# Kernel optimization log

Hardware: AMD Instinct MI355X
Metric: run time of the kernel (lower is better)

## Reference

```python
import jax, jax.numpy as jnp
import numpy as np

N = 4096
IN_C = 256
F = 256          # num_filter
C = 40           # label_dim
KP1 = 3          # K+1 Chebyshev orders (K=2 hardcoded in forward)
E = 131072
TWO_PI = 2.0 * np.pi


def build_Lc(edges, q, edge_weight, n):
    """Conjugate of the normalized magnetic Laplacian (max_eigen=2 => L = -A_n * exp(i*Theta)).
    We return conj(L) because the original code swaps L.real/L.imag when feeding `process`,
    which is algebraically O_i = i * conj(T_i(L))."""
    row, col = edges[0], edges[1]
    A = jnp.zeros((n, n), jnp.float32).at[row, col].add(edge_weight)  # duplicates sum, as in coo_matrix
    A_sym = 0.5 * (A + A.T)
    d = A_sym.sum(axis=0)
    d = jnp.where(d == 0, 1.0, d)
    dinv = d ** -0.5
    A_n = dinv[:, None] * A_sym * dinv[None, :]
    Theta = TWO_PI * q * (A - A.T)
    # conj(L) = -A_n * exp(-i*Theta)
    return (-A_n).astype(jnp.complex64) * jnp.exp(-1j * Theta.astype(jnp.complex64))


def cheb_layer(Lc, Xr, Xi, W, b):
    """One ChebConv_Qin_Direct layer. Output = sum_i (i * T_i(conj(L)) @ Xc) @ W_i + bias,
    which reproduces the real/imag-swapped `process` of the original module."""
    Xc = (Xr + 1j * Xi).astype(jnp.complex64)      # [N, d]
    Z0 = Xc
    Z1 = Lc @ Xc                                   # sparse-equivalent spmm, dense here
    Z2 = 2.0 * (Lc @ Z1) - Z0                      # Chebyshev recursion T2 = 2 L T1 - T0
    Yc = 1j * (Z0 @ W[0].astype(jnp.complex64)
               + Z1 @ W[1].astype(jnp.complex64)
               + Z2 @ W[2].astype(jnp.complex64))  # [N, out]
    return Yc.real + b, Yc.imag + b


def setup_inputs() -> dict:
    key = jax.random.key(0)
    k = jax.random.split(key, 8)
    stdv1 = 1.0 / np.sqrt(F)
    return {
        "real": jax.random.normal(k[0], (N, IN_C), jnp.float32),
        "imag": jax.random.normal(k[1], (N, IN_C), jnp.float32),
        "edges": jax.random.randint(k[2], (2, E), 0, N),
        "q": jnp.float32(0.25),
        "edge_weight": jax.random.uniform(k[3], (E,), jnp.float32),
        "W1": jax.random.uniform(k[4], (KP1, IN_C, F), jnp.float32, -stdv1, stdv1),
        "b1": jnp.zeros((1, F), jnp.float32),
        "W2": jax.random.uniform(k[5], (KP1, F, F), jnp.float32, -stdv1, stdv1),
        "b2": jnp.zeros((1, F), jnp.float32),
        "Wc": jax.random.normal(k[6], (C, 2 * F), jnp.float32) * (1.0 / np.sqrt(2 * F)),
        "bc": jnp.zeros((C,), jnp.float32),
    }


def reference(real, imag, edges, q, edge_weight, W1, b1, W2, b2, Wc, bc):
    n = real.shape[0]
    Lc = build_Lc(edges, q, edge_weight, n)        # same L is rebuilt each layer in the original
    r, i = cheb_layer(Lc, real, imag, W1, b1)
    r, i = cheb_layer(Lc, r, i, W2, b2)            # activation=False, dropout=False
    x = jnp.concatenate([r, i], axis=-1)           # [N, 2F]
    logits = x @ Wc.T + bc                         # Conv1d(kernel_size=1) == linear
    return jax.nn.log_softmax(logits, axis=-1)     # [N, C]
```

## Files before the change

### kernel.cpp

```cpp
#include <hip/hip_runtime.h>
#include <cmath>

#define N_NODES 4096
#define FDIM    256
#define CDIM    40
#define NEDGE   131072
#define CAP     256
#define HBITS   20
#define HSIZE   (1 << HBITS)
#define TWO_PI_F 6.28318530717958647692f

typedef __bf16 bf16;
typedef __bf16 bf16x2 __attribute__((ext_vector_type(2)));
typedef __bf16 bf16x4 __attribute__((ext_vector_type(4)));
typedef __bf16 bf16x8 __attribute__((ext_vector_type(8)));
typedef float  f32x4  __attribute__((ext_vector_type(4)));

static constexpr size_t NF = (size_t)N_NODES * FDIM;

struct __align__(16) Entry { float lr, li; int col, pad; };

__device__ __forceinline__ void gld_lds16(const bf16* g, bf16* s) {
    __builtin_amdgcn_global_load_lds(
        (const __attribute__((address_space(1))) void*)g,
        (__attribute__((address_space(3))) void*)s,
        16, 0, 0);
}

__device__ __forceinline__ unsigned cell_hash(unsigned cell) {
    return (cell * 2654435761u) >> (32 - HBITS);
}

__global__ void hash_insert(const int* __restrict__ edges,
                            const float* __restrict__ ew,
                            int* __restrict__ hkey, float* __restrict__ hval,
                            float* __restrict__ rowsum, float* __restrict__ colsum) {
    int e = blockIdx.x * blockDim.x + threadIdx.x;
    if (e >= NEDGE) return;
    int r = edges[e], c = edges[NEDGE + e];
    float wv = ew[e];
    atomicAdd(rowsum + r, wv);
    atomicAdd(colsum + c, wv);
    unsigned cell = (unsigned)r * N_NODES + c;
    unsigned h = cell_hash(cell);
    for (;;) {
        int old = atomicCAS(hkey + h, 0, (int)(cell + 1));
        if (old == 0 || old == (int)(cell + 1)) { atomicAdd(hval + h, wv); break; }
        h = (h + 1) & (HSIZE - 1);
    }
}

__global__ void dinv_k(const float* __restrict__ rowsum,
                       const float* __restrict__ colsum,
                       float* __restrict__ dinv) {
    int j = blockIdx.x * blockDim.x + threadIdx.x;
    if (j < N_NODES) {
        float d = 0.5f * (rowsum[j] + colsum[j]);
        if (d == 0.f) d = 1.f;
        dinv[j] = 1.0f / sqrtf(d);
    }
}

__global__ __launch_bounds__(256) void hash_to_ell(
    const int* __restrict__ hkey, const float* __restrict__ hval,
    const float* __restrict__ dinv, const float* __restrict__ qptr,
    int* __restrict__ cnt, Entry* __restrict__ ent) {
    int h = blockIdx.x * 256 + threadIdx.x;
    int k = hkey[h];
    if (k == 0) return;
    unsigned cell = (unsigned)(k - 1);
    int i = cell >> 12, j = cell & 4095;
    float a = hval[h];
    float b = 0.f;
    bool mirror = false;
    if (i == j) { b = a; mirror = true; }
    else {
        unsigned mcell = (unsigned)j * N_NODES + i;
        unsigned hh = cell_hash(mcell);
        for (;;) {
            int kk = hkey[hh];
            if (kk == (int)(mcell + 1)) { b = hval[hh]; mirror = true; break; }
            if (kk == 0) break;
            hh = (hh + 1) & (HSIZE - 1);
        }
    }
    float an = 0.5f * (a + b) * dinv[i] * dinv[j];
    float s, c;
    sincosf(TWO_PI_F * qptr[0] * (a - b), &s, &c);
    int pos = atomicAdd(cnt + i, 1);
    if (pos < CAP) {
        Entry en; en.lr = -an * c; en.li = an * s; en.col = j; en.pad = 0;
        ent[(size_t)i * CAP + pos] = en;
    }
    if (!mirror) {
        int pos2 = atomicAdd(cnt + j, 1);
        if (pos2 < CAP) {
            Entry en; en.lr = -an * c; en.li = -an * s; en.col = i; en.pad = 0;
            ent[(size_t)j * CAP + pos2] = en;
        }
    }
}

__global__ __launch_bounds__(256) void cast_in2(const float* __restrict__ Xr,
                                                const float* __restrict__ Xi,
                                                bf16* __restrict__ Xr16,
                                                bf16* __restrict__ Xi16,
                                                bf16* __restrict__ XC) {
    int idx = blockIdx.x * 256 + threadIdx.x;
    float vr = Xr[idx], vi = Xi[idx];
    Xr16[idx] = (bf16)vr; Xi16[idx] = (bf16)vi;
    bf16x2 p; p[0] = (bf16)vr; p[1] = (bf16)vi;
    ((bf16x2*)XC)[idx] = p;
}

__global__ __launch_bounds__(256) void cast_w(const float* __restrict__ W,
                                              bf16* __restrict__ Wt) {
    int idx = blockIdx.x * 256 + threadIdx.x;
    if (idx < 256 * 768) {
        int nout = idx / 768, kk = idx - nout * 768;
        int o = kk >> 8, k = kk & 255;
        Wt[idx] = (bf16)W[((size_t)o * 256 + k) * 256 + nout];
    }
}

__global__ __launch_bounds__(256) void cast_wc(const float* __restrict__ Wc,
                                               bf16* __restrict__ Wcb) {
    int idx = blockIdx.x * 256 + threadIdx.x;
    int row = idx >> 9, k = idx & 511;
    Wcb[idx] = (row < CDIM) ? (bf16)Wc[row * 512 + k] : (bf16)0.f;
}

__global__ __launch_bounds__(256) void spmm_k(
    const int* __restrict__ cnt, const Entry* __restrict__ ent,
    const bf16* __restrict__ XC,
    const bf16* __restrict__ C0C,
    float alpha, float beta,
    bf16* __restrict__ Zr, bf16* __restrict__ Zi, bf16* __restrict__ ZC)
{
    __shared__ f32x4 redR[3][64];
    __shared__ f32x4 redI[3][64];

    const int wave = threadIdx.x >> 6, lane = threadIdx.x & 63;
    const int row = blockIdx.x;
    int n1 = cnt[row]; if (n1 > CAP) n1 = CAP;
    const Entry* erow = ent + (size_t)row * CAP;

    float ar[4] = {}, ai[4] = {};
    int e = wave;
    for (; e + 4 < n1; e += 8) {
        Entry e0 = erow[e];
        Entry e1 = erow[e + 4];
        bf16x8 x0 = *(const bf16x8*)&XC[(size_t)(e0.col & 4095) * 512 + lane * 8];
        bf16x8 x1 = *(const bf16x8*)&XC[(size_t)(e1.col & 4095) * 512 + lane * 8];
        #pragma unroll
        for (int c = 0; c < 4; ++c) {
            float xr0 = (float)x0[2 * c], xi0 = (float)x0[2 * c + 1];
            ar[c] += e0.lr * xr0 - e0.li * xi0;
            ai[c] += e0.lr * xi0 + e0.li * xr0;
            float xr1 = (float)x1[2 * c], xi1 = (float)x1[2 * c + 1];
            ar[c] += e1.lr * xr1 - e1.li * xi1;
            ai[c] += e1.lr * xi1 + e1.li * xr1;
        }
    }
    if (e < n1) {
        Entry e0 = erow[e];
        bf16x8 x0 = *(const bf16x8*)&XC[(size_t)(e0.col & 4095) * 512 + lane * 8];
        #pragma unroll
        for (int c = 0; c < 4; ++c) {
            float xr0 = (float)x0[2 * c], xi0 = (float)x0[2 * c + 1];
            ar[c] += e0.lr * xr0 - e0.li * xi0;
            ai[c] += e0.lr * xi0 + e0.li * xr0;
        }
    }

    if (wave != 0) {
        f32x4 r, i;
        #pragma unroll
        for (int c = 0; c < 4; ++c) { r[c] = ar[c]; i[c] = ai[c]; }
        redR[wave - 1][lane] = r;
        redI[wave - 1][lane] = i;
    }
    __syncthreads();
    if (wave != 0) return;

    #pragma unroll
    for (int w = 0; w < 3; ++w) {
        f32x4 r = redR[w][lane], i = redI[w][lane];
        #pragma unroll
        for (int c = 0; c < 4; ++c) { ar[c] += r[c]; ai[c] += i[c]; }
    }

    float vr[4], vi[4];
    if (beta != 0.f) {
        bf16x8 c0 = *(const bf16x8*)&C0C[(size_t)row * 512 + lane * 8];
        #pragma unroll
        for (int c = 0; c < 4; ++c) {
            vr[c] = alpha * ar[c] + beta * (float)c0[2 * c];
            vi[c] = alpha * ai[c] + beta * (float)c0[2 * c + 1];
        }
    } else {
        #pragma unroll
        for (int c = 0; c < 4; ++c) { vr[c] = alpha * ar[c]; vi[c] = alpha * ai[c]; }
    }
    size_t base = (size_t)row * FDIM + lane * 4;
    bf16x4 pr, pi;
    #pragma unroll
    for (int c = 0; c < 4; ++c) { pr[c] = (bf16)vr[c]; pi[c] = (bf16)vi[c]; }
    *(bf16x4*)&Zr[base] = pr;
    *(bf16x4*)&Zi[base] = pi;
    if (ZC) {
        bf16x8 o;
        #pragma unroll
        for (int c = 0; c < 4; ++c) { o[2 * c] = pr[c]; o[2 * c + 1] = pi[c]; }
        *(bf16x8*)&ZC[(size_t)row * 512 + lane * 8] = o;
    }
}

__global__ __launch_bounds__(256) void wapply_mfma(
    const bf16* __restrict__ Z0r, const bf16* __restrict__ Z0i,
    const bf16* __restrict__ Z1r, const bf16* __restrict__ Z1i,
    const bf16* __restrict__ Z2r, const bf16* __restrict__ Z2i,
    const bf16* __restrict__ Wt,
    const float* __restrict__ bias,
    float* __restrict__ O32r, float* __restrict__ O32i,
    bf16* __restrict__ O16r_r, bf16* __restrict__ O16r_i,
    bf16* __restrict__ OC)
{
    __shared__ __align__(16) bf16 sZr[64 * 32];
    __shared__ __align__(16) bf16 sZi[64 * 32];
    __shared__ __align__(16) bf16 sW [64 * 32];

    const int tid  = threadIdx.x;
    const int wave = tid >> 6;
    const int lane = tid & 63;
    const int rowBase = blockIdx.y * 64;
    const int colBase = blockIdx.x * 64;

    const int srow = lane >> 2;
    const int skc  = (lane & 3) * 8;

    f32x4 accSr[2][2] = {}, accSi[2][2] = {};
    const int wm = wave & 1, wn = wave >> 1;
    const int fr = lane & 15;
    const int fk = (lane >> 4) * 8;

    for (int kb = 0; kb < 3 * FDIM; kb += 32) {
        int order = kb >> 8;
        int kloc  = kb & 255;
        if (wave == 0 || wave == 1) {
            const bf16* z;
            if (wave == 0) z = (order == 0) ? Z0r : (order == 1) ? Z1r : Z2r;
            else           z = (order == 0) ? Z0i : (order == 1) ? Z1i : Z2i;
            bf16* s = (wave == 0) ? sZr : sZi;
            const bf16* g = z + (size_t)(rowBase + srow) * FDIM + kloc + skc;
            #pragma unroll
            for (int t = 0; t < 4; ++t)
                gld_lds16(g + (size_t)t * 16 * FDIM, s + t * 512);
        } else if (wave == 2) {
            const bf16* g = Wt + (size_t)(colBase + srow) * 768 + kb + skc;
            #pragma unroll
            for (int t = 0; t < 4; ++t)
                gld_lds16(g + (size_t)t * 16 * 768, sW + t * 512);
        }
        __syncthreads();

        bf16x8 zr[2], zi[2], wv[2];
        #pragma unroll
        for (int m = 0; m < 2; ++m) {
            int r = wm * 32 + m * 16 + fr;
            zr[m] = *(const bf16x8*)&sZr[r * 32 + fk];
            zi[m] = *(const bf16x8*)&sZi[r * 32 + fk];
        }
        #pragma unroll
        for (int n = 0; n < 2; ++n) {
            int c = wn * 32 + n * 16 + fr;
            wv[n] = *(const bf16x8*)&sW[c * 32 + fk];
        }
        #pragma unroll
        for (int m = 0; m < 2; ++m)
            #pragma unroll
            for (int n = 0; n < 2; ++n) {
                accSr[m][n] = __builtin_amdgcn_mfma_f32_16x16x32_bf16(zr[m], wv[n], accSr[m][n], 0, 0, 0);
                accSi[m][n] = __builtin_amdgcn_mfma_f32_16x16x32_bf16(zi[m], wv[n], accSi[m][n], 0, 0, 0);
            }
        __syncthreads();
    }

    #pragma unroll
    for (int m = 0; m < 2; ++m)
        #pragma unroll
        for (int n = 0; n < 2; ++n) {
            int row0 = rowBase + wm * 32 + m * 16 + (lane >> 4) * 4;
            int col  = colBase + wn * 32 + n * 16 + (lane & 15);
            float bv = bias[col];
            #pragma unroll
            for (int r = 0; r < 4; ++r) {
                float vr = bv - accSi[m][n][r];
                float vi = bv + accSr[m][n][r];
                int row = row0 + r;
                size_t idx = (size_t)row * FDIM + col;
                if (O32r) {
                    O32r[idx] = vr; O32i[idx] = vi;
                }
                if (O16r_r) {
                    O16r_r[idx] = (bf16)vr; O16r_i[idx] = (bf16)vi;
                }
                if (OC) {
                    bf16x2 p; p[0] = (bf16)vr; p[1] = (bf16)vi;
                    ((bf16x2*)OC)[idx] = p;
                }
            }
        }
}

__global__ __launch_bounds__(256) void head_mfma(
    const bf16* __restrict__ Yrb,
    const bf16* __restrict__ Yib,
    const bf16* __restrict__ Wcb,
    const float* __restrict__ bc,
    float* __restrict__ out)
{
    __shared__ __align__(16) bf16 sY[64][72];
    __shared__ __align__(16) bf16 sW[48][72];
    __shared__ float sS[64][52];

    const int tid  = threadIdx.x;
    const int wave = tid >> 6;
    const int lane = tid & 63;
    const int r0 = blockIdx.x * 64;

    f32x4 acc[3] = {};

    for (int kb = 0; kb < 512; kb += 64) {
        const bf16* src = (kb < 256) ? Yrb : Yib;
        const int koff = kb & 255;
        #pragma unroll
        for (int e = 0; e < 2; ++e) {
            int idx = tid + e * 256;
            int rr = idx >> 3, kk = (idx & 7) * 8;
            *(bf16x8*)&sY[rr][kk] =
                *(const bf16x8*)&src[(size_t)(r0 + rr) * FDIM + koff + kk];
        }
        #pragma unroll
        for (int e = 0; e < 2; ++e) {
            int idx = tid + e * 256;
            if (idx < 384) {
                int rr = idx >> 3, kk = (idx & 7) * 8;
                *(bf16x8*)&sW[rr][kk] =
                    *(const bf16x8*)&Wcb[(size_t)rr * 512 + kb + kk];
            }
        }
        __syncthreads();
        #pragma unroll
        for (int ks = 0; ks < 2; ++ks) {
            bf16x8 a = *(const bf16x8*)&sY[wave * 16 + (lane & 15)][ks * 32 + (lane >> 4) * 8];
            #pragma unroll
            for (int n = 0; n < 3; ++n) {
                bf16x8 b = *(const bf16x8*)&sW[n * 16 + (lane & 15)][ks * 32 + (lane >> 4) * 8];
                acc[n] = __builtin_amdgcn_mfma_f32_16x16x32_bf16(a, b, acc[n], 0, 0, 0);
            }
        }
        __syncthreads();
    }

    #pragma unroll
    for (int n = 0; n < 3; ++n) {
        int col = n * 16 + (lane & 15);
        int rloc = wave * 16 + (lane >> 4) * 4;
        #pragma unroll
        for (int r = 0; r < 4; ++r)
            sS[rloc + r][col] = acc[n][r];
    }
    __syncthreads();

    if (tid < 64) {
        float mx = -INFINITY;
        #pragma unroll 8
        for (int c = 0; c < CDIM; ++c) {
            float lv = sS[tid][c] + bc[c];
            sS[tid][c] = lv;
            mx = fmaxf(mx, lv);
        }
        float se = 0.f;
        #pragma unroll 8
        for (int c = 0; c < CDIM; ++c) se += expf(sS[tid][c] - mx);
        float lse = mx + logf(se);
        #pragma unroll 8
        for (int c = 0; c < CDIM; ++c)
            out[(size_t)(r0 + tid) * CDIM + c] = sS[tid][c] - lse;
    }
}

extern "C" void kernel_launch(void* const* d_in, const int* in_sizes, int n_in,
                              void* d_out, int out_size, void* d_ws, size_t ws_size,
                              hipStream_t stream) {
    const float* real = (const float*)d_in[0];
    const float* imag = (const float*)d_in[1];
    const int*   edges = (const int*)d_in[2];
    const float* q    = (const float*)d_in[3];
    const float* ew   = (const float*)d_in[4];
    const float* W1   = (const float*)d_in[5];
    const float* b1   = (const float*)d_in[6];
    const float* W2   = (const float*)d_in[7];
    const float* b2   = (const float*)d_in[8];
    const float* Wc   = (const float*)d_in[9];
    const float* bc   = (const float*)d_in[10];
    float* out = (float*)d_out;

    char* w = (char*)d_ws;
    int*      hkey   = (int*)w;   w += (size_t)HSIZE * 4;
    float*    hval   = (float*)w; w += (size_t)HSIZE * 4;
    int*      cnt    = (int*)w;   w += N_NODES * 4;
    float*    rowsum = (float*)w; w += N_NODES * 4;
    float*    colsum = (float*)w; w += N_NODES * 4;
    size_t zero_bytes = (size_t)((char*)w - (char*)d_ws);
    Entry* ent  = (Entry*)w; w += (size_t)N_NODES * CAP * 16;
    float* dinv = (float*)w; w += N_NODES * 4;
    bf16* Xr16 = (bf16*)w; w += NF * 2;
    bf16* Xi16 = (bf16*)w; w += NF * 2;
    bf16* XC   = (bf16*)w; w += NF * 4;
    bf16* Z1r  = (bf16*)w; w += NF * 2;
    bf16* Z1i  = (bf16*)w; w += NF * 2;
    bf16* Z1C  = (bf16*)w; w += NF * 4;
    bf16* Z2r  = (bf16*)w; w += NF * 2;
    bf16* Z2i  = (bf16*)w; w += NF * 2;
    float* Y1r32 = (float*)w; w += NF * 4;
    float* Y1i32 = (float*)w; w += NF * 4;
    bf16* Y1rb = (bf16*)w; w += NF * 2;
    bf16* Y1ib = (bf16*)w; w += NF * 2;
    bf16* Y1C  = (bf16*)w; w += NF * 4;
    bf16* Y2rb = (bf16*)w; w += NF * 2;
    bf16* Y2ib = (bf16*)w; w += NF * 2;
    bf16* W1t  = (bf16*)w; w += 256 * 768 * 2;
    bf16* W2t  = (bf16*)w; w += 256 * 768 * 2;
    bf16* Wcb  = (bf16*)w; w += 48 * 512 * 2;

    hipMemsetAsync(d_ws, 0, zero_bytes, stream);

    hash_insert<<<(NEDGE + 255) / 256, 256, 0, stream>>>(edges, ew, hkey, hval,
                                                         rowsum, colsum);
    dinv_k<<<16, 256, 0, stream>>>(rowsum, colsum, dinv);
    hash_to_ell<<<HSIZE / 256, 256, 0, stream>>>(hkey, hval, dinv, q, cnt, ent);

    cast_in2<<<NF / 256, 256, 0, stream>>>(real, imag, Xr16, Xi16, XC);
    cast_w<<<768, 256, 0, stream>>>(W1, W1t);
    cast_w<<<768, 256, 0, stream>>>(W2, W2t);
    cast_wc<<<96, 256, 0, stream>>>(Wc, Wcb);

    dim3 gW(FDIM / 64, N_NODES / 64);

    spmm_k<<<N_NODES, 256, 0, stream>>>(cnt, ent, XC, nullptr,
                                        1.f, 0.f, Z1r, Z1i, Z1C);
    spmm_k<<<N_NODES, 256, 0, stream>>>(cnt, ent, Z1C, XC,
                                        2.f, -1.f, Z2r, Z2i, nullptr);
    wapply_mfma<<<gW, 256, 0, stream>>>(Xr16, Xi16, Z1r, Z1i, Z2r, Z2i,
                                        W1t, b1,
                                        Y1r32, Y1i32,
                                        Y1rb, Y1ib,
                                        Y1C);

    spmm_k<<<N_NODES, 256, 0, stream>>>(cnt, ent, Y1C, nullptr,
                                        1.f, 0.f, Z1r, Z1i, Z1C);
    spmm_k<<<N_NODES, 256, 0, stream>>>(cnt, ent, Z1C, Y1C,
                                        2.f, -1.f, Z2r, Z2i, nullptr);
    wapply_mfma<<<gW, 256, 0, stream>>>(Y1rb, Y1ib, Z1r, Z1i, Z2r, Z2i,
                                        W2t, b2,
                                        nullptr, nullptr,
                                        Y2rb, Y2ib,
                                        nullptr);

    head_mfma<<<64, 256, 0, stream>>>(Y2rb, Y2ib, Wcb, bc, out);
}
```

Measured before the change: 279.8 us.

## Fold dinv into hash_to_ell, merge weight casts, unroll spmm gather by four

Result: faster. 272.7 us (-2.5%).

```diff
diff --git a/kernel.cpp b/kernel.cpp
--- a/kernel.cpp
+++ b/kernel.cpp
@@ -50,20 +50,10 @@
     }
 }
 
-__global__ void dinv_k(const float* __restrict__ rowsum,
-                       const float* __restrict__ colsum,
-                       float* __restrict__ dinv) {
-    int j = blockIdx.x * blockDim.x + threadIdx.x;
-    if (j < N_NODES) {
-        float d = 0.5f * (rowsum[j] + colsum[j]);
-        if (d == 0.f) d = 1.f;
-        dinv[j] = 1.0f / sqrtf(d);
-    }
-}
-
 __global__ __launch_bounds__(256) void hash_to_ell(
     const int* __restrict__ hkey, const float* __restrict__ hval,
-    const float* __restrict__ dinv, const float* __restrict__ qptr,
+    const float* __restrict__ rowsum, const float* __restrict__ colsum,
+    const float* __restrict__ qptr,
     int* __restrict__ cnt, Entry* __restrict__ ent) {
     int h = blockIdx.x * 256 + threadIdx.x;
     int k = hkey[h];
@@ -84,7 +74,9 @@
             hh = (hh + 1) & (HSIZE - 1);
         }
     }
-    float an = 0.5f * (a + b) * dinv[i] * dinv[j];
+    float di = 0.5f * (rowsum[i] + colsum[i]); if (di == 0.f) di = 1.f;
+    float dj = 0.5f * (rowsum[j] + colsum[j]); if (dj == 0.f) dj = 1.f;
+    float an = 0.5f * (a + b) / sqrtf(di * dj);
     float s, c;
     sincosf(TWO_PI_F * qptr[0] * (a - b), &s, &c);
     int pos = atomicAdd(cnt + i, 1);
@@ -113,21 +105,26 @@
     ((bf16x2*)XC)[idx] = p;
 }
 
-__global__ __launch_bounds__(256) void cast_w(const float* __restrict__ W,
-                                              bf16* __restrict__ Wt) {
+#define NWT (256 * 768)
+__global__ __launch_bounds__(256) void cast_weights(
+    const float* __restrict__ W1, const float* __restrict__ W2,
+    const float* __restrict__ Wc,
+    bf16* __restrict__ W1t, bf16* __restrict__ W2t, bf16* __restrict__ Wcb) {
     int idx = blockIdx.x * 256 + threadIdx.x;
-    if (idx < 256 * 768) {
-        int nout = idx / 768, kk = idx - nout * 768;
+    if (idx < 2 * NWT) {
+        const float* W = (idx < NWT) ? W1 : W2;
+        bf16* Wt = (idx < NWT) ? W1t : W2t;
+        int id = (idx < NWT) ? idx : idx - NWT;
+        int nout = id / 768, kk = id - nout * 768;
         int o = kk >> 8, k = kk & 255;
-        Wt[idx] = (bf16)W[((size_t)o * 256 + k) * 256 + nout];
-    }
-}
-
-__global__ __launch_bounds__(256) void cast_wc(const float* __restrict__ Wc,
-                                               bf16* __restrict__ Wcb) {
-    int idx = blockIdx.x * 256 + threadIdx.x;
-    int row = idx >> 9, k = idx & 511;
-    Wcb[idx] = (row < CDIM) ? (bf16)Wc[row * 512 + k] : (bf16)0.f;
+        Wt[id] = (bf16)W[((size_t)o * 256 + k) * 256 + nout];
+    } else {
+        int id = idx - 2 * NWT;
+        if (id < 48 * 512) {
+            int row = id >> 9, k = id & 511;
+            Wcb[id] = (row < CDIM) ? (bf16)Wc[row * 512 + k] : (bf16)0.f;
+        }
+    }
 }
 
 __global__ __launch_bounds__(256) void spmm_k(
@@ -147,22 +144,29 @@
 
     float ar[4] = {}, ai[4] = {};
     int e = wave;
-    for (; e + 4 < n1; e += 8) {
+    for (; e + 12 < n1; e += 16) {
         Entry e0 = erow[e];
         Entry e1 = erow[e + 4];
+        Entry e2 = erow[e + 8];
+        Entry e3 = erow[e + 12];
         bf16x8 x0 = *(const bf16x8*)&XC[(size_t)(e0.col & 4095) * 512 + lane * 8];
         bf16x8 x1 = *(const bf16x8*)&XC[(size_t)(e1.col & 4095) * 512 + lane * 8];
+        bf16x8 x2 = *(const bf16x8*)&XC[(size_t)(e2.col & 4095) * 512 + lane * 8];
+        bf16x8 x3 = *(const bf16x8*)&XC[(size_t)(e3.col & 4095) * 512 + lane * 8];
         #pragma unroll
         for (int c = 0; c < 4; ++c) {
-            float xr0 = (float)x0[2 * c], xi0 = (float)x0[2 * c + 1];
-            ar[c] += e0.lr * xr0 - e0.li * xi0;
-            ai[c] += e0.lr * xi0 + e0.li * xr0;
-            float xr1 = (float)x1[2 * c], xi1 = (float)x1[2 * c + 1];
-            ar[c] += e1.lr * xr1 - e1.li * xi1;
-            ai[c] += e1.lr * xi1 + e1.li * xr1;
-        }
-    }
-    if (e < n1) {
+            float xr, xi;
+            xr = (float)x0[2 * c]; xi = (float)x0[2 * c + 1];
+            ar[c] += e0.lr * xr - e0.li * xi;  ai[c] += e0.lr * xi + e0.li * xr;
+            xr = (float)x1[2 * c]; xi = (float)x1[2 * c + 1];
+            ar[c] += e1.lr * xr - e1.li * xi;  ai[c] += e1.lr * xi + e1.li * xr;
+            xr = (float)x2[2 * c]; xi = (float)x2[2 * c + 1];
+            ar[c] += e2.lr * xr - e2.li * xi;  ai[c] += e2.lr * xi + e2.li * xr;
+            xr = (float)x3[2 * c]; xi = (float)x3[2 * c + 1];
+            ar[c] += e3.lr * xr - e3.li * xi;  ai[c] += e3.lr * xi + e3.li * xr;
+        }
+    }
+    for (; e < n1; e += 4) {
         Entry e0 = erow[e];
         bf16x8 x0 = *(const bf16x8*)&XC[(size_t)(e0.col & 4095) * 512 + lane * 8];
         #pragma unroll
@@ -415,7 +419,6 @@
     float*    colsum = (float*)w; w += N_NODES * 4;
     size_t zero_bytes = (size_t)((char*)w - (char*)d_ws);
     Entry* ent  = (Entry*)w; w += (size_t)N_NODES * CAP * 16;
-    float* dinv = (float*)w; w += N_NODES * 4;
     bf16* Xr16 = (bf16*)w; w += NF * 2;
     bf16* Xi16 = (bf16*)w; w += NF * 2;
     bf16* XC   = (bf16*)w; w += NF * 4;
@@ -439,13 +442,12 @@
 
     hash_insert<<<(NEDGE + 255) / 256, 256, 0, stream>>>(edges, ew, hkey, hval,
                                                          rowsum, colsum);
-    dinv_k<<<16, 256, 0, stream>>>(rowsum, colsum, dinv);
-    hash_to_ell<<<HSIZE / 256, 256, 0, stream>>>(hkey, hval, dinv, q, cnt, ent);
+    hash_to_ell<<<HSIZE / 256, 256, 0, stream>>>(hkey, hval, rowsum, colsum,
+                                                 q, cnt, ent);
 
     cast_in2<<<NF / 256, 256, 0, stream>>>(real, imag, Xr16, Xi16, XC);
-    cast_w<<<768, 256, 0, stream>>>(W1, W1t);
-    cast_w<<<768, 256, 0, stream>>>(W2, W2t);
-    cast_wc<<<96, 256, 0, stream>>>(Wc, Wcb);
+    cast_weights<<<(2 * NWT + 48 * 512 + 255) / 256, 256, 0, stream>>>(
+        W1, W2, Wc, W1t, W2t, Wcb);
 
     dim3 gW(FDIM / 64, N_NODES / 64);
 
```
